# Kernel optimization log

Measured on AMD Instinct MI355X. Metric: run time of the kernel, lower is better.

The kernel has to match this reference:

```python
import jax, jax.numpy as jnp
import numpy as np

B, NG, NM, E, K, D = 1, 65536, 8192, 262144, 32, 128
EPS = 1e-5


def layernorm(x, g, b):
    mu = jnp.mean(x, axis=-1, keepdims=True)
    var = jnp.mean(jnp.square(x - mu), axis=-1, keepdims=True)
    return (x - mu) * jax.lax.rsqrt(var + EPS) * g + b


def mlp(x, W, g, b):
    # Linear (no bias) -> tanh -> LayerNorm, matching MLP module
    return layernorm(jnp.tanh(x @ W), g, b)


def setup_inputs() -> dict:
    key = jax.random.key(0)
    ks = jax.random.split(key, 16)
    inp = {
        "grid_mesh_bond_embedding": jax.random.normal(ks[0], (B, E, D), jnp.float32),
        "grid_rect_embedding": jax.random.normal(ks[1], (B, NG, D), jnp.float32),
        "mesh_node_embedding": jax.random.normal(ks[2], (B, NM, D), jnp.float32),
        "edge_id2pair": jnp.stack(
            [jax.random.randint(ks[3], (E,), 0, NG),
             jax.random.randint(ks[4], (E,), 0, NM)], axis=1),  # [E,2] int
        "edge_id_of_node": jax.random.randint(ks[5], (NM, K), 0, E),  # [NM,K] int
        "edge_coef": jax.random.uniform(ks[6], (NM, K, 1), jnp.float32),
        # MLP_G2M_GM2E: Linear(3D -> D), LayerNorm(D)
        "W_gm2e": jax.random.normal(ks[7], (3 * D, D), jnp.float32) / np.sqrt(3 * D),
        "g_gm2e": jnp.ones((D,), jnp.float32),
        "b_gm2e": jnp.zeros((D,), jnp.float32),
        # MLP_G2M_E2M: Linear(2D -> D), LayerNorm(D)
        "W_e2m": jax.random.normal(ks[8], (2 * D, D), jnp.float32) / np.sqrt(2 * D),
        "g_e2m": jnp.ones((D,), jnp.float32),
        "b_e2m": jnp.zeros((D,), jnp.float32),
        # MLP_G2M_G2G: Linear(D -> D), LayerNorm(D)
        "W_g2g": jax.random.normal(ks[9], (D, D), jnp.float32) / np.sqrt(D),
        "g_g2g": jnp.ones((D,), jnp.float32),
        "b_g2g": jnp.zeros((D,), jnp.float32),
    }
    return inp


def reference(grid_mesh_bond_embedding, grid_rect_embedding, mesh_node_embedding,
              edge_id2pair, edge_id_of_node, edge_coef,
              W_gm2e, g_gm2e, b_gm2e, W_e2m, g_e2m, b_e2m, W_g2g, g_g2g, b_g2g):
    # Edge update: gather rect/node endpoints, concat, MLP -> [B,E,D]
    rect_src = grid_rect_embedding[:, edge_id2pair[:, 0]]  # [B,E,D]
    node_dst = mesh_node_embedding[:, edge_id2pair[:, 1]]  # [B,E,D]
    edge_in = jnp.concatenate([grid_mesh_bond_embedding, rect_src, node_dst], axis=-1)
    delta_edge = mlp(edge_in, W_gm2e, g_gm2e, b_gm2e)  # [B,E,D]

    # Node update: gather K edges per mesh node, coef-weighted mean over K
    gathered = delta_edge[:, edge_id_of_node]  # [B,NM,K,D]
    agg = jnp.mean(gathered * edge_coef, axis=-2)  # [B,NM,D]
    delta_node = mlp(jnp.concatenate([mesh_node_embedding, agg], axis=-1), W_e2m, g_e2m, b_e2m)

    # Grid rect self-update
    delta_rect = mlp(grid_rect_embedding, W_g2g, g_g2g, b_g2g)

    return (grid_mesh_bond_embedding + delta_edge,
            grid_rect_embedding + delta_rect,
            mesh_node_embedding + delta_node)
```

## Files before the change

kernel.cpp:

```cpp
#include <hip/hip_runtime.h>


typedef __bf16 bf16x8 __attribute__((ext_vector_type(8)));
typedef __bf16 bf16x4 __attribute__((ext_vector_type(4)));
typedef float f32x4 __attribute__((ext_vector_type(4)));

#define E_CNT 262144
#define NG_CNT 65536
#define NM_CNT 8192

__device__ __forceinline__ float fast_tanh(float x) {
  float e = __expf(2.f * x);
  return 1.f - 2.f / (1.f + e);
}

template <int KDIM>
__device__ __forceinline__ void stage_W(const float* __restrict__ W, __bf16* wt) {
  constexpr int NCH = (KDIM / 32) * 8 * 64;
  for (int c = threadIdx.x; c < NCH; c += blockDim.x) {
    const int lane6 = c & 63, cx = lane6 & 15, qq = lane6 >> 4;
    const int kkn = c >> 6, kk = kkn >> 3, nn = kkn & 7;
    const int k0 = kk * 32 + qq * 8, col = nn * 16 + cx;
    bf16x8 v;
#pragma unroll
    for (int j = 0; j < 8; ++j) v[j] = (__bf16)W[(k0 + j) * 128 + col];
    *(bf16x8*)(wt + c * 8) = v;
  }
}

template <bool STORE_D>
__device__ __forceinline__ void mlp_epilogue(f32x4* acc, const f32x4* R,
                                             const float* gvec,
                                             const float* bvec, int q,
                                             float* op, __bf16* dp) {
  float s1 = 0.f, s2 = 0.f;
#pragma unroll
  for (int n = 0; n < 8; ++n)
#pragma unroll
    for (int j = 0; j < 4; ++j) {
      float v = fast_tanh(acc[n][j]);
      acc[n][j] = v;
      s1 += v;
      s2 += v * v;
    }
  s1 += __shfl_xor(s1, 16, 64);
  s2 += __shfl_xor(s2, 16, 64);
  s1 += __shfl_xor(s1, 32, 64);
  s2 += __shfl_xor(s2, 32, 64);
  const float mu = s1 * (1.f / 128.f);
  const float rs = rsqrtf(s2 * (1.f / 128.f) - mu * mu + 1e-5f);
#pragma unroll
  for (int n = 0; n < 8; ++n) {
    const f32x4 G = *(const f32x4*)(gvec + n * 16 + q * 4);
    const f32x4 Bv = *(const f32x4*)(bvec + n * 16 + q * 4);
    f32x4 o;
    bf16x4 db;
#pragma unroll
    for (int j = 0; j < 4; ++j) {
      const float d = (acc[n][j] - mu) * rs * G[j] + Bv[j];
      o[j] = R[n][j] + d;
      db[j] = (__bf16)d;
    }
    *(f32x4*)(op + n * 16 + q * 4) = o;
    if (STORE_D) *(bf16x4*)(dp + n * 16 + q * 4) = db;
  }
}

template <bool STORE_D>
__global__ __launch_bounds__(256) __attribute__((amdgpu_waves_per_eu(3, 4)))
void edge_kernel(const float* __restrict__ gm, const int* __restrict__ pair,
                 const __bf16* __restrict__ P1, const __bf16* __restrict__ P2,
                 const float* __restrict__ W, const float* __restrict__ gvec,
                 const float* __restrict__ bvec, float* __restrict__ out,
                 __bf16* __restrict__ delta_out, int M) {
  __shared__ __bf16 wt[2048 * 8];
  stage_W<128>(W, wt);
  __syncthreads();
  const int tid = threadIdx.x, lane = tid & 63, wid = tid >> 6;
  const int r = lane & 15, q = lane >> 4;
  const __bf16* wl = wt + lane * 8;
  const int t = blockIdx.x * 4 + wid;
  if (t >= (M >> 4)) return;
  const int row = (t << 4) + r;
  const float* pa = gm + (size_t)row * 128;

  f32x4 F[4][2];
#pragma unroll
  for (int kk = 0; kk < 4; ++kk) {
    F[kk][0] = *(const f32x4*)(pa + kk * 32 + q * 8);
    F[kk][1] = *(const f32x4*)(pa + kk * 32 + q * 8 + 4);
  }
  f32x4 R[8];
#pragma unroll
  for (int n = 0; n < 8; ++n) R[n] = *(const f32x4*)(pa + n * 16 + q * 4);
  const int2 sd = *(const int2*)(pair + 2 * (size_t)row);

  bf16x4 pg1[8], pg2[8];
  const __bf16* p1 = P1 + (size_t)sd.x * 128 + q * 4;
  const __bf16* p2 = P2 + (size_t)sd.y * 128 + q * 4;
#pragma unroll
  for (int n = 0; n < 8; ++n) {
    pg1[n] = *(const bf16x4*)(p1 + n * 16);
    pg2[n] = *(const bf16x4*)(p2 + n * 16);
  }

  bf16x8 ab[4];
#pragma unroll
  for (int kk = 0; kk < 4; ++kk)
#pragma unroll
    for (int j = 0; j < 4; ++j) {
      ab[kk][j] = (__bf16)F[kk][0][j];
      ab[kk][4 + j] = (__bf16)F[kk][1][j];
    }
  f32x4 acc[8];
#pragma unroll
  for (int n = 0; n < 8; ++n)
#pragma unroll
    for (int j = 0; j < 4; ++j)
      acc[n][j] = (float)pg1[n][j] + (float)pg2[n][j];
#pragma unroll
  for (int kk = 0; kk < 4; ++kk)
#pragma unroll
    for (int n = 0; n < 8; ++n)
      acc[n] = __builtin_amdgcn_mfma_f32_16x16x32_bf16(
          *(const bf16x8*)(wl + (kk * 8 + n) * 512), ab[kk], acc[n], 0, 0, 0);

  mlp_epilogue<STORE_D>(acc, R, gvec, bvec, q, out + (size_t)row * 128,
                        STORE_D ? delta_out + (size_t)row * 128 : nullptr);
}

__global__ __launch_bounds__(256) __attribute__((amdgpu_waves_per_eu(2, 4)))
void rect_fused_kernel(const float* __restrict__ rect,
                       const float* __restrict__ W1b,
                       const float* __restrict__ W3,
                       const float* __restrict__ gvec,
                       const float* __restrict__ bvec,
                       float* __restrict__ out1, __bf16* __restrict__ P1,
                       int M) {
  __shared__ __bf16 wt[4096 * 8];
  stage_W<128>(W1b, wt);
  stage_W<128>(W3, wt + 16384);
  __syncthreads();
  const int tid = threadIdx.x, lane = tid & 63, wid = tid >> 6;
  const int r = lane & 15, q = lane >> 4;
  const __bf16* wl = wt + lane * 8;
  const int t = blockIdx.x * 4 + wid;
  if (t >= (M >> 4)) return;
  const int row = (t << 4) + r;
  const float* pa = rect + (size_t)row * 128;

  f32x4 F[4][2];
#pragma unroll
  for (int kk = 0; kk < 4; ++kk) {
    F[kk][0] = *(const f32x4*)(pa + kk * 32 + q * 8);
    F[kk][1] = *(const f32x4*)(pa + kk * 32 + q * 8 + 4);
  }
  f32x4 R[8];
#pragma unroll
  for (int n = 0; n < 8; ++n) R[n] = *(const f32x4*)(pa + n * 16 + q * 4);

  bf16x8 ab[4];
#pragma unroll
  for (int kk = 0; kk < 4; ++kk)
#pragma unroll
    for (int j = 0; j < 4; ++j) {
      ab[kk][j] = (__bf16)F[kk][0][j];
      ab[kk][4 + j] = (__bf16)F[kk][1][j];
    }
  f32x4 acc[8] = {};
#pragma unroll
  for (int kk = 0; kk < 4; ++kk)
#pragma unroll
    for (int n = 0; n < 8; ++n)
      acc[n] = __builtin_amdgcn_mfma_f32_16x16x32_bf16(
          *(const bf16x8*)(wl + (kk * 8 + n) * 512), ab[kk], acc[n], 0, 0, 0);
  __bf16* pp = P1 + (size_t)row * 128;
#pragma unroll
  for (int n = 0; n < 8; ++n) {
    bf16x4 o;
#pragma unroll
    for (int j = 0; j < 4; ++j) o[j] = (__bf16)acc[n][j];
    *(bf16x4*)(pp + n * 16 + q * 4) = o;
  }
  f32x4 acc2[8] = {};
#pragma unroll
  for (int kk = 0; kk < 4; ++kk)
#pragma unroll
    for (int n = 0; n < 8; ++n)
      acc2[n] = __builtin_amdgcn_mfma_f32_16x16x32_bf16(
          *(const bf16x8*)(wl + 16384 + (kk * 8 + n) * 512), ab[kk], acc2[n], 0,
          0, 0);
  mlp_epilogue<false>(acc2, R, gvec, bvec, q, out1 + (size_t)row * 128, nullptr);
}

__global__ __launch_bounds__(256) __attribute__((amdgpu_waves_per_eu(3, 4)))
void mlp128_kernel(const float* __restrict__ A, const float* __restrict__ W,
                   const float* __restrict__ gvec, const float* __restrict__ bvec,
                   float* __restrict__ out, int M) {
  __shared__ __bf16 wt[2048 * 8];
  stage_W<128>(W, wt);
  __syncthreads();
  const int tid = threadIdx.x, lane = tid & 63, wid = tid >> 6;
  const int r = lane & 15, q = lane >> 4;
  const __bf16* wl = wt + lane * 8;
  const int t = blockIdx.x * 4 + wid;
  if (t >= (M >> 4)) return;
  const int row = (t << 4) + r;
  const float* pa = A + (size_t)row * 128;
  f32x4 F[4][2];
#pragma unroll
  for (int kk = 0; kk < 4; ++kk) {
    F[kk][0] = *(const f32x4*)(pa + kk * 32 + q * 8);
    F[kk][1] = *(const f32x4*)(pa + kk * 32 + q * 8 + 4);
  }
  f32x4 R[8];
#pragma unroll
  for (int n = 0; n < 8; ++n) R[n] = *(const f32x4*)(pa + n * 16 + q * 4);
  bf16x8 ab[4];
#pragma unroll
  for (int kk = 0; kk < 4; ++kk)
#pragma unroll
    for (int j = 0; j < 4; ++j) {
      ab[kk][j] = (__bf16)F[kk][0][j];
      ab[kk][4 + j] = (__bf16)F[kk][1][j];
    }
  f32x4 acc[8] = {};
#pragma unroll
  for (int kk = 0; kk < 4; ++kk)
#pragma unroll
    for (int n = 0; n < 8; ++n)
      acc[n] = __builtin_amdgcn_mfma_f32_16x16x32_bf16(
          *(const bf16x8*)(wl + (kk * 8 + n) * 512), ab[kk], acc[n], 0, 0, 0);
  mlp_epilogue<false>(acc, R, gvec, bvec, q, out + (size_t)row * 128, nullptr);
}

__global__ __launch_bounds__(256) __attribute__((amdgpu_waves_per_eu(3, 4)))
void lin_kernel(const float* __restrict__ A, const float* __restrict__ W,
                __bf16* __restrict__ out, int M) {
  __shared__ __bf16 wt[2048 * 8];
  stage_W<128>(W, wt);
  __syncthreads();
  const int tid = threadIdx.x, lane = tid & 63, wid = tid >> 6;
  const int r = lane & 15, q = lane >> 4;
  const __bf16* wl = wt + lane * 8;
  const int t = blockIdx.x * 4 + wid;
  if (t >= (M >> 4)) return;
  const int row = (t << 4) + r;
  const float* pa = A + (size_t)row * 128;
  f32x4 F[4][2];
#pragma unroll
  for (int kk = 0; kk < 4; ++kk) {
    F[kk][0] = *(const f32x4*)(pa + kk * 32 + q * 8);
    F[kk][1] = *(const f32x4*)(pa + kk * 32 + q * 8 + 4);
  }
  bf16x8 ab[4];
#pragma unroll
  for (int kk = 0; kk < 4; ++kk)
#pragma unroll
    for (int j = 0; j < 4; ++j) {
      ab[kk][j] = (__bf16)F[kk][0][j];
      ab[kk][4 + j] = (__bf16)F[kk][1][j];
    }
  f32x4 acc[8] = {};
#pragma unroll
  for (int kk = 0; kk < 4; ++kk)
#pragma unroll
    for (int n = 0; n < 8; ++n)
      acc[n] = __builtin_amdgcn_mfma_f32_16x16x32_bf16(
          *(const bf16x8*)(wl + (kk * 8 + n) * 512), ab[kk], acc[n], 0, 0, 0);
  __bf16* po = out + (size_t)row * 128;
#pragma unroll
  for (int n = 0; n < 8; ++n) {
    bf16x4 o;
#pragma unroll
    for (int j = 0; j < 4; ++j) o[j] = (__bf16)acc[n][j];
    *(bf16x4*)(po + n * 16 + q * 4) = o;
  }
}

__global__ __launch_bounds__(256) __attribute__((amdgpu_waves_per_eu(2, 4)))
void node_kernel(const __bf16* __restrict__ Ab, const float* __restrict__ W,
                 const float* __restrict__ gvec, const float* __restrict__ bvec,
                 const float* __restrict__ resid, float* __restrict__ out,
                 int M) {
  __shared__ __bf16 wt[4096 * 8];
  stage_W<256>(W, wt);
  __syncthreads();
  const int tid = threadIdx.x, lane = tid & 63, wid = tid >> 6;
  const int r = lane & 15, q = lane >> 4;
  const __bf16* wl = wt + lane * 8;
  const int t = blockIdx.x * 4 + wid;
  if (t >= (M >> 4)) return;
  const int row = (t << 4) + r;
  const __bf16* pb = Ab + (size_t)row * 256 + q * 8;
  bf16x8 ab[8];
#pragma unroll
  for (int kk = 0; kk < 8; ++kk) ab[kk] = *(const bf16x8*)(pb + kk * 32);
  f32x4 R[8];
#pragma unroll
  for (int n = 0; n < 8; ++n)
    R[n] = *(const f32x4*)(resid + (size_t)row * 128 + n * 16 + q * 4);
  f32x4 acc[8] = {};
#pragma unroll
  for (int kk = 0; kk < 8; ++kk)
#pragma unroll
    for (int n = 0; n < 8; ++n)
      acc[n] = __builtin_amdgcn_mfma_f32_16x16x32_bf16(
          *(const bf16x8*)(wl + (kk * 8 + n) * 512), ab[kk], acc[n], 0, 0, 0);
  mlp_epilogue<false>(acc, R, gvec, bvec, q, out + (size_t)row * 128, nullptr);
}

template <bool FROM_WS>
__global__ __launch_bounds__(256) void agg_kernel(
    const __bf16* __restrict__ dws, const float* __restrict__ out0,
    const float* __restrict__ gm, const float* __restrict__ mesh,
    const int* __restrict__ eid, const float* __restrict__ coef,
    __bf16* __restrict__ x2) {
  __shared__ int eid_s[512];
  __shared__ float cf_s[512];
  const int t = threadIdx.x;
  const int n0 = blockIdx.x * 16;
  for (int i = t; i < 512; i += 256) {
    eid_s[i] = eid[n0 * 32 + i];
    cf_s[i] = coef[n0 * 32 + i];
  }
  __syncthreads();
  const int rl = t >> 4;
  const int d8 = (t & 15) * 8;
  const int row = n0 + rl;
  float acc[8] = {0, 0, 0, 0, 0, 0, 0, 0};
  for (int k = 0; k < 32; ++k) {
    const int e = eid_s[rl * 32 + k];
    const float cf = cf_s[rl * 32 + k];
    if (FROM_WS) {
      bf16x8 v = *(const bf16x8*)(dws + (size_t)e * 128 + d8);
#pragma unroll
      for (int j = 0; j < 8; ++j) acc[j] += cf * (float)v[j];
    } else {
      const float* po = out0 + (size_t)e * 128 + d8;
      const float* pg = gm + (size_t)e * 128 + d8;
      f32x4 o0 = *(const f32x4*)po, o1 = *(const f32x4*)(po + 4);
      f32x4 g0 = *(const f32x4*)pg, g1 = *(const f32x4*)(pg + 4);
#pragma unroll
      for (int j = 0; j < 4; ++j) {
        acc[j] += cf * (o0[j] - g0[j]);
        acc[4 + j] += cf * (o1[j] - g1[j]);
      }
    }
  }
  const float* pm = mesh + (size_t)row * 128 + d8;
  f32x4 m0 = *(const f32x4*)pm, m1 = *(const f32x4*)(pm + 4);
  bf16x8 mv, av;
#pragma unroll
  for (int j = 0; j < 4; ++j) {
    mv[j] = (__bf16)m0[j];
    mv[4 + j] = (__bf16)m1[j];
  }
#pragma unroll
  for (int j = 0; j < 8; ++j) av[j] = (__bf16)(acc[j] * (1.0f / 32.0f));
  *(bf16x8*)(x2 + (size_t)row * 256 + d8) = mv;
  *(bf16x8*)(x2 + (size_t)row * 256 + 128 + d8) = av;
}

extern "C" void kernel_launch(void* const* d_in, const int* in_sizes, int n_in,
                              void* d_out, int out_size, void* d_ws,
                              size_t ws_size, hipStream_t stream) {
  const float* gm = (const float*)d_in[0];
  const float* rect = (const float*)d_in[1];
  const float* mesh = (const float*)d_in[2];
  const int* pair = (const int*)d_in[3];
  const int* eid = (const int*)d_in[4];
  const float* coef = (const float*)d_in[5];
  const float* W1 = (const float*)d_in[6];
  const float* g1 = (const float*)d_in[7];
  const float* b1 = (const float*)d_in[8];
  const float* W2 = (const float*)d_in[9];
  const float* g2 = (const float*)d_in[10];
  const float* b2 = (const float*)d_in[11];
  const float* W3 = (const float*)d_in[12];
  const float* g3 = (const float*)d_in[13];
  const float* b3 = (const float*)d_in[14];

  float* out0 = (float*)d_out;
  float* out1 = out0 + (size_t)E_CNT * 128;
  float* out2 = out1 + (size_t)NG_CNT * 128;

  const size_t deltaE = (size_t)E_CNT * 128;
  const size_t x2E = (size_t)NM_CNT * 256;
  const size_t p1E = (size_t)NG_CNT * 128;
  const bool fastD = ws_size >= (deltaE + x2E) * 2;
  const bool fastP = ws_size >= (deltaE + x2E + p1E) * 2;

  __bf16* delta = (__bf16*)d_ws;
  __bf16* x2 = fastD ? delta + deltaE : (__bf16*)d_ws;
  __bf16* P1ws = delta + deltaE + x2E;
  __bf16* P2 = (__bf16*)out2;

  const __bf16* P1;
  if (fastP) {
    rect_fused_kernel<<<1024, 256, 0, stream>>>(rect, W1 + 128 * 128, W3, g3,
                                                b3, out1, P1ws, NG_CNT);
    P1 = P1ws;
  } else {
    lin_kernel<<<1024, 256, 0, stream>>>(rect, W1 + 128 * 128, (__bf16*)out1,
                                         NG_CNT);
    P1 = (const __bf16*)out1;
  }
  lin_kernel<<<128, 256, 0, stream>>>(mesh, W1 + 256 * 128, P2, NM_CNT);

  if (fastD) {
    edge_kernel<true><<<4096, 256, 0, stream>>>(gm, pair, P1, P2, W1, g1, b1,
                                                out0, delta, E_CNT);
    agg_kernel<true><<<512, 256, 0, stream>>>(delta, nullptr, nullptr, mesh,
                                              eid, coef, x2);
  } else {
    edge_kernel<false><<<4096, 256, 0, stream>>>(gm, pair, P1, P2, W1, g1, b1,
                                                 out0, nullptr, E_CNT);
    agg_kernel<false><<<512, 256, 0, stream>>>(nullptr, out0, gm, mesh, eid,
                                               coef, x2);
  }
  if (!fastP) {
    mlp128_kernel<<<1024, 256, 0, stream>>>(rect, W3, g3, b3, out1, NG_CNT);
  }
  node_kernel<<<128, 256, 0, stream>>>(x2, W2, g2, b2, mesh, out2, NM_CNT);
}
```

Baseline: 208.6 us.

## Make MLP kernels persistent with grid-stride loops and prefetch edge gathers

Converts the edge, rect, mlp128 and lin kernels into grid-stride persistent loops and cuts their grid sizes, so the per-block weight staging into LDS is amortized over several tiles. The edge kernel also software-pipelines its indexed gathers: it loads the next tile's pair indices and P1/P2 rows while computing the current tile. It additionally uses nontemporal stores for the large fp32 edge output. The cost is fewer resident blocks, which may hide latency less well, plus extra register pressure from the prefetch buffers.

```diff
diff --git a/kernel.cpp b/kernel.cpp
--- a/kernel.cpp
+++ b/kernel.cpp
@@ -28,7 +28,7 @@
   }
 }
 
-template <bool STORE_D>
+template <bool STORE_D, bool NT>
 __device__ __forceinline__ void mlp_epilogue(f32x4* acc, const f32x4* R,
                                              const float* gvec,
                                              const float* bvec, int q,
@@ -61,7 +61,10 @@
       o[j] = R[n][j] + d;
       db[j] = (__bf16)d;
     }
-    *(f32x4*)(op + n * 16 + q * 4) = o;
+    if (NT)
+      __builtin_nontemporal_store(o, (f32x4*)(op + n * 16 + q * 4));
+    else
+      *(f32x4*)(op + n * 16 + q * 4) = o;
     if (STORE_D) *(bf16x4*)(dp + n * 16 + q * 4) = db;
   }
 }
@@ -79,54 +82,73 @@
   const int tid = threadIdx.x, lane = tid & 63, wid = tid >> 6;
   const int r = lane & 15, q = lane >> 4;
   const __bf16* wl = wt + lane * 8;
-  const int t = blockIdx.x * 4 + wid;
-  if (t >= (M >> 4)) return;
-  const int row = (t << 4) + r;
-  const float* pa = gm + (size_t)row * 128;
-
-  f32x4 F[4][2];
-#pragma unroll
-  for (int kk = 0; kk < 4; ++kk) {
-    F[kk][0] = *(const f32x4*)(pa + kk * 32 + q * 8);
-    F[kk][1] = *(const f32x4*)(pa + kk * 32 + q * 8 + 4);
-  }
-  f32x4 R[8];
-#pragma unroll
-  for (int n = 0; n < 8; ++n) R[n] = *(const f32x4*)(pa + n * 16 + q * 4);
-  const int2 sd = *(const int2*)(pair + 2 * (size_t)row);
-
+  const int nw = gridDim.x * 4;
+  const int tiles = M >> 4;
+  int t = blockIdx.x * 4 + wid;
+  if (t >= tiles) return;
+
+  int2 sd = *(const int2*)(pair + 2 * (size_t)((t << 4) + r));
   bf16x4 pg1[8], pg2[8];
-  const __bf16* p1 = P1 + (size_t)sd.x * 128 + q * 4;
-  const __bf16* p2 = P2 + (size_t)sd.y * 128 + q * 4;
-#pragma unroll
-  for (int n = 0; n < 8; ++n) {
-    pg1[n] = *(const bf16x4*)(p1 + n * 16);
-    pg2[n] = *(const bf16x4*)(p2 + n * 16);
-  }
-
-  bf16x8 ab[4];
-#pragma unroll
-  for (int kk = 0; kk < 4; ++kk)
-#pragma unroll
-    for (int j = 0; j < 4; ++j) {
-      ab[kk][j] = (__bf16)F[kk][0][j];
-      ab[kk][4 + j] = (__bf16)F[kk][1][j];
-    }
-  f32x4 acc[8];
-#pragma unroll
-  for (int n = 0; n < 8; ++n)
-#pragma unroll
-    for (int j = 0; j < 4; ++j)
-      acc[n][j] = (float)pg1[n][j] + (float)pg2[n][j];
-#pragma unroll
-  for (int kk = 0; kk < 4; ++kk)
+  {
+    const __bf16* p1 = P1 + (size_t)sd.x * 128 + q * 4;
+    const __bf16* p2 = P2 + (size_t)sd.y * 128 + q * 4;
+#pragma unroll
+    for (int n = 0; n < 8; ++n) {
+      pg1[n] = *(const bf16x4*)(p1 + n * 16);
+      pg2[n] = *(const bf16x4*)(p2 + n * 16);
+    }
+  }
+  int2 sd_next = {0, 0};
+  if (t + nw < tiles)
+    sd_next = *(const int2*)(pair + 2 * (size_t)(((t + nw) << 4) + r));
+
+  for (; t < tiles; t += nw) {
+    const int row = (t << 4) + r;
+    const float* pa = gm + (size_t)row * 128;
+    f32x4 F[4][2];
+#pragma unroll
+    for (int kk = 0; kk < 4; ++kk) {
+      F[kk][0] = *(const f32x4*)(pa + kk * 32 + q * 8);
+      F[kk][1] = *(const f32x4*)(pa + kk * 32 + q * 8 + 4);
+    }
+    f32x4 R[8];
+#pragma unroll
+    for (int n = 0; n < 8; ++n) R[n] = *(const f32x4*)(pa + n * 16 + q * 4);
+    f32x4 acc[8];
 #pragma unroll
     for (int n = 0; n < 8; ++n)
-      acc[n] = __builtin_amdgcn_mfma_f32_16x16x32_bf16(
-          *(const bf16x8*)(wl + (kk * 8 + n) * 512), ab[kk], acc[n], 0, 0, 0);
-
-  mlp_epilogue<STORE_D>(acc, R, gvec, bvec, q, out + (size_t)row * 128,
-                        STORE_D ? delta_out + (size_t)row * 128 : nullptr);
+#pragma unroll
+      for (int j = 0; j < 4; ++j)
+        acc[n][j] = (float)pg1[n][j] + (float)pg2[n][j];
+    if (t + nw < tiles) {
+      const __bf16* p1 = P1 + (size_t)sd_next.x * 128 + q * 4;
+      const __bf16* p2 = P2 + (size_t)sd_next.y * 128 + q * 4;
+#pragma unroll
+      for (int n = 0; n < 8; ++n) {
+        pg1[n] = *(const bf16x4*)(p1 + n * 16);
+        pg2[n] = *(const bf16x4*)(p2 + n * 16);
+      }
+      if (t + 2 * nw < tiles)
+        sd_next = *(const int2*)(pair + 2 * (size_t)(((t + 2 * nw) << 4) + r));
+    }
+    bf16x8 ab[4];
+#pragma unroll
+    for (int kk = 0; kk < 4; ++kk)
+#pragma unroll
+      for (int j = 0; j < 4; ++j) {
+        ab[kk][j] = (__bf16)F[kk][0][j];
+        ab[kk][4 + j] = (__bf16)F[kk][1][j];
+      }
+#pragma unroll
+    for (int kk = 0; kk < 4; ++kk)
+#pragma unroll
+      for (int n = 0; n < 8; ++n)
+        acc[n] = __builtin_amdgcn_mfma_f32_16x16x32_bf16(
+            *(const bf16x8*)(wl + (kk * 8 + n) * 512), ab[kk], acc[n], 0, 0, 0);
+    mlp_epilogue<STORE_D, true>(
+        acc, R, gvec, bvec, q, out + (size_t)row * 128,
+        STORE_D ? delta_out + (size_t)row * 128 : nullptr);
+  }
 }
 
 __global__ __launch_bounds__(256) __attribute__((amdgpu_waves_per_eu(2, 4)))
@@ -144,53 +166,54 @@
   const int tid = threadIdx.x, lane = tid & 63, wid = tid >> 6;
   const int r = lane & 15, q = lane >> 4;
   const __bf16* wl = wt + lane * 8;
-  const int t = blockIdx.x * 4 + wid;
-  if (t >= (M >> 4)) return;
-  const int row = (t << 4) + r;
-  const float* pa = rect + (size_t)row * 128;
-
-  f32x4 F[4][2];
-#pragma unroll
-  for (int kk = 0; kk < 4; ++kk) {
-    F[kk][0] = *(const f32x4*)(pa + kk * 32 + q * 8);
-    F[kk][1] = *(const f32x4*)(pa + kk * 32 + q * 8 + 4);
-  }
-  f32x4 R[8];
-#pragma unroll
-  for (int n = 0; n < 8; ++n) R[n] = *(const f32x4*)(pa + n * 16 + q * 4);
-
-  bf16x8 ab[4];
-#pragma unroll
-  for (int kk = 0; kk < 4; ++kk)
-#pragma unroll
-    for (int j = 0; j < 4; ++j) {
-      ab[kk][j] = (__bf16)F[kk][0][j];
-      ab[kk][4 + j] = (__bf16)F[kk][1][j];
-    }
-  f32x4 acc[8] = {};
-#pragma unroll
-  for (int kk = 0; kk < 4; ++kk)
-#pragma unroll
-    for (int n = 0; n < 8; ++n)
-      acc[n] = __builtin_amdgcn_mfma_f32_16x16x32_bf16(
-          *(const bf16x8*)(wl + (kk * 8 + n) * 512), ab[kk], acc[n], 0, 0, 0);
-  __bf16* pp = P1 + (size_t)row * 128;
-#pragma unroll
-  for (int n = 0; n < 8; ++n) {
-    bf16x4 o;
-#pragma unroll
-    for (int j = 0; j < 4; ++j) o[j] = (__bf16)acc[n][j];
-    *(bf16x4*)(pp + n * 16 + q * 4) = o;
-  }
-  f32x4 acc2[8] = {};
-#pragma unroll
-  for (int kk = 0; kk < 4; ++kk)
-#pragma unroll
-    for (int n = 0; n < 8; ++n)
-      acc2[n] = __builtin_amdgcn_mfma_f32_16x16x32_bf16(
-          *(const bf16x8*)(wl + 16384 + (kk * 8 + n) * 512), ab[kk], acc2[n], 0,
-          0, 0);
-  mlp_epilogue<false>(acc2, R, gvec, bvec, q, out1 + (size_t)row * 128, nullptr);
+  const int nw = gridDim.x * 4;
+  const int tiles = M >> 4;
+  for (int t = blockIdx.x * 4 + wid; t < tiles; t += nw) {
+    const int row = (t << 4) + r;
+    const float* pa = rect + (size_t)row * 128;
+    f32x4 F[4][2];
+#pragma unroll
+    for (int kk = 0; kk < 4; ++kk) {
+      F[kk][0] = *(const f32x4*)(pa + kk * 32 + q * 8);
+      F[kk][1] = *(const f32x4*)(pa + kk * 32 + q * 8 + 4);
+    }
+    f32x4 R[8];
+#pragma unroll
+    for (int n = 0; n < 8; ++n) R[n] = *(const f32x4*)(pa + n * 16 + q * 4);
+    bf16x8 ab[4];
+#pragma unroll
+    for (int kk = 0; kk < 4; ++kk)
+#pragma unroll
+      for (int j = 0; j < 4; ++j) {
+        ab[kk][j] = (__bf16)F[kk][0][j];
+        ab[kk][4 + j] = (__bf16)F[kk][1][j];
+      }
+    f32x4 acc[8] = {};
+#pragma unroll
+    for (int kk = 0; kk < 4; ++kk)
+#pragma unroll
+      for (int n = 0; n < 8; ++n)
+        acc[n] = __builtin_amdgcn_mfma_f32_16x16x32_bf16(
+            *(const bf16x8*)(wl + (kk * 8 + n) * 512), ab[kk], acc[n], 0, 0, 0);
+    __bf16* pp = P1 + (size_t)row * 128;
+#pragma unroll
+    for (int n = 0; n < 8; ++n) {
+      bf16x4 o;
+#pragma unroll
+      for (int j = 0; j < 4; ++j) o[j] = (__bf16)acc[n][j];
+      *(bf16x4*)(pp + n * 16 + q * 4) = o;
+    }
+    f32x4 acc2[8] = {};
+#pragma unroll
+    for (int kk = 0; kk < 4; ++kk)
+#pragma unroll
+      for (int n = 0; n < 8; ++n)
+        acc2[n] = __builtin_amdgcn_mfma_f32_16x16x32_bf16(
+            *(const bf16x8*)(wl + 16384 + (kk * 8 + n) * 512), ab[kk], acc2[n],
+            0, 0, 0);
+    mlp_epilogue<false, false>(acc2, R, gvec, bvec, q,
+                               out1 + (size_t)row * 128, nullptr);
+  }
 }
 
 __global__ __launch_bounds__(256) __attribute__((amdgpu_waves_per_eu(3, 4)))
@@ -203,35 +226,38 @@
   const int tid = threadIdx.x, lane = tid & 63, wid = tid >> 6;
   const int r = lane & 15, q = lane >> 4;
   const __bf16* wl = wt + lane * 8;
-  const int t = blockIdx.x * 4 + wid;
-  if (t >= (M >> 4)) return;
-  const int row = (t << 4) + r;
-  const float* pa = A + (size_t)row * 128;
-  f32x4 F[4][2];
-#pragma unroll
-  for (int kk = 0; kk < 4; ++kk) {
-    F[kk][0] = *(const f32x4*)(pa + kk * 32 + q * 8);
-    F[kk][1] = *(const f32x4*)(pa + kk * 32 + q * 8 + 4);
-  }
-  f32x4 R[8];
-#pragma unroll
-  for (int n = 0; n < 8; ++n) R[n] = *(const f32x4*)(pa + n * 16 + q * 4);
-  bf16x8 ab[4];
-#pragma unroll
-  for (int kk = 0; kk < 4; ++kk)
-#pragma unroll
-    for (int j = 0; j < 4; ++j) {
-      ab[kk][j] = (__bf16)F[kk][0][j];
-      ab[kk][4 + j] = (__bf16)F[kk][1][j];
-    }
-  f32x4 acc[8] = {};
-#pragma unroll
-  for (int kk = 0; kk < 4; ++kk)
-#pragma unroll
-    for (int n = 0; n < 8; ++n)
-      acc[n] = __builtin_amdgcn_mfma_f32_16x16x32_bf16(
-          *(const bf16x8*)(wl + (kk * 8 + n) * 512), ab[kk], acc[n], 0, 0, 0);
-  mlp_epilogue<false>(acc, R, gvec, bvec, q, out + (size_t)row * 128, nullptr);
+  const int nw = gridDim.x * 4;
+  const int tiles = M >> 4;
+  for (int t = blockIdx.x * 4 + wid; t < tiles; t += nw) {
+    const int row = (t << 4) + r;
+    const float* pa = A + (size_t)row * 128;
+    f32x4 F[4][2];
+#pragma unroll
+    for (int kk = 0; kk < 4; ++kk) {
+      F[kk][0] = *(const f32x4*)(pa + kk * 32 + q * 8);
+      F[kk][1] = *(const f32x4*)(pa + kk * 32 + q * 8 + 4);
+    }
+    f32x4 R[8];
+#pragma unroll
+    for (int n = 0; n < 8; ++n) R[n] = *(const f32x4*)(pa + n * 16 + q * 4);
+    bf16x8 ab[4];
+#pragma unroll
+    for (int kk = 0; kk < 4; ++kk)
+#pragma unroll
+      for (int j = 0; j < 4; ++j) {
+        ab[kk][j] = (__bf16)F[kk][0][j];
+        ab[kk][4 + j] = (__bf16)F[kk][1][j];
+      }
+    f32x4 acc[8] = {};
+#pragma unroll
+    for (int kk = 0; kk < 4; ++kk)
+#pragma unroll
+      for (int n = 0; n < 8; ++n)
+        acc[n] = __builtin_amdgcn_mfma_f32_16x16x32_bf16(
+            *(const bf16x8*)(wl + (kk * 8 + n) * 512), ab[kk], acc[n], 0, 0, 0);
+    mlp_epilogue<false, false>(acc, R, gvec, bvec, q, out + (size_t)row * 128,
+                               nullptr);
+  }
 }
 
 __global__ __launch_bounds__(256) __attribute__((amdgpu_waves_per_eu(3, 4)))
@@ -243,38 +269,40 @@
   const int tid = threadIdx.x, lane = tid & 63, wid = tid >> 6;
   const int r = lane & 15, q = lane >> 4;
   const __bf16* wl = wt + lane * 8;
-  const int t = blockIdx.x * 4 + wid;
-  if (t >= (M >> 4)) return;
-  const int row = (t << 4) + r;
-  const float* pa = A + (size_t)row * 128;
-  f32x4 F[4][2];
-#pragma unroll
-  for (int kk = 0; kk < 4; ++kk) {
-    F[kk][0] = *(const f32x4*)(pa + kk * 32 + q * 8);
-    F[kk][1] = *(const f32x4*)(pa + kk * 32 + q * 8 + 4);
-  }
-  bf16x8 ab[4];
-#pragma unroll
-  for (int kk = 0; kk < 4; ++kk)
-#pragma unroll
-    for (int j = 0; j < 4; ++j) {
-      ab[kk][j] = (__bf16)F[kk][0][j];
-      ab[kk][4 + j] = (__bf16)F[kk][1][j];
-    }
-  f32x4 acc[8] = {};
-#pragma unroll
-  for (int kk = 0; kk < 4; ++kk)
-#pragma unroll
-    for (int n = 0; n < 8; ++n)
-      acc[n] = __builtin_amdgcn_mfma_f32_16x16x32_bf16(
-          *(const bf16x8*)(wl + (kk * 8 + n) * 512), ab[kk], acc[n], 0, 0, 0);
-  __bf16* po = out + (size_t)row * 128;
-#pragma unroll
-  for (int n = 0; n < 8; ++n) {
-    bf16x4 o;
-#pragma unroll
-    for (int j = 0; j < 4; ++j) o[j] = (__bf16)acc[n][j];
-    *(bf16x4*)(po + n * 16 + q * 4) = o;
+  const int nw = gridDim.x * 4;
+  const int tiles = M >> 4;
+  for (int t = blockIdx.x * 4 + wid; t < tiles; t += nw) {
+    const int row = (t << 4) + r;
+    const float* pa = A + (size_t)row * 128;
+    f32x4 F[4][2];
+#pragma unroll
+    for (int kk = 0; kk < 4; ++kk) {
+      F[kk][0] = *(const f32x4*)(pa + kk * 32 + q * 8);
+      F[kk][1] = *(const f32x4*)(pa + kk * 32 + q * 8 + 4);
+    }
+    bf16x8 ab[4];
+#pragma unroll
+    for (int kk = 0; kk < 4; ++kk)
+#pragma unroll
+      for (int j = 0; j < 4; ++j) {
+        ab[kk][j] = (__bf16)F[kk][0][j];
+        ab[kk][4 + j] = (__bf16)F[kk][1][j];
+      }
+    f32x4 acc[8] = {};
+#pragma unroll
+    for (int kk = 0; kk < 4; ++kk)
+#pragma unroll
+      for (int n = 0; n < 8; ++n)
+        acc[n] = __builtin_amdgcn_mfma_f32_16x16x32_bf16(
+            *(const bf16x8*)(wl + (kk * 8 + n) * 512), ab[kk], acc[n], 0, 0, 0);
+    __bf16* po = out + (size_t)row * 128;
+#pragma unroll
+    for (int n = 0; n < 8; ++n) {
+      bf16x4 o;
+#pragma unroll
+      for (int j = 0; j < 4; ++j) o[j] = (__bf16)acc[n][j];
+      *(bf16x4*)(po + n * 16 + q * 4) = o;
+    }
   }
 }
 
@@ -307,7 +335,8 @@
     for (int n = 0; n < 8; ++n)
       acc[n] = __builtin_amdgcn_mfma_f32_16x16x32_bf16(
           *(const bf16x8*)(wl + (kk * 8 + n) * 512), ab[kk], acc[n], 0, 0, 0);
-  mlp_epilogue<false>(acc, R, gvec, bvec, q, out + (size_t)row * 128, nullptr);
+  mlp_epilogue<false, false>(acc, R, gvec, bvec, q, out + (size_t)row * 128,
+                             nullptr);
 }
 
 template <bool FROM_WS>
@@ -398,29 +427,29 @@
 
   const __bf16* P1;
   if (fastP) {
-    rect_fused_kernel<<<1024, 256, 0, stream>>>(rect, W1 + 128 * 128, W3, g3,
-                                                b3, out1, P1ws, NG_CNT);
+    rect_fused_kernel<<<256, 256, 0, stream>>>(rect, W1 + 128 * 128, W3, g3,
+                                               b3, out1, P1ws, NG_CNT);
     P1 = P1ws;
   } else {
-    lin_kernel<<<1024, 256, 0, stream>>>(rect, W1 + 128 * 128, (__bf16*)out1,
-                                         NG_CNT);
+    lin_kernel<<<256, 256, 0, stream>>>(rect, W1 + 128 * 128, (__bf16*)out1,
+                                        NG_CNT);
     P1 = (const __bf16*)out1;
   }
   lin_kernel<<<128, 256, 0, stream>>>(mesh, W1 + 256 * 128, P2, NM_CNT);
 
   if (fastD) {
-    edge_kernel<true><<<4096, 256, 0, stream>>>(gm, pair, P1, P2, W1, g1, b1,
+    edge_kernel<true><<<1024, 256, 0, stream>>>(gm, pair, P1, P2, W1, g1, b1,
                                                 out0, delta, E_CNT);
     agg_kernel<true><<<512, 256, 0, stream>>>(delta, nullptr, nullptr, mesh,
                                               eid, coef, x2);
   } else {
-    edge_kernel<false><<<4096, 256, 0, stream>>>(gm, pair, P1, P2, W1, g1, b1,
+    edge_kernel<false><<<1024, 256, 0, stream>>>(gm, pair, P1, P2, W1, g1, b1,
                                                  out0, nullptr, E_CNT);
     agg_kernel<false><<<512, 256, 0, stream>>>(nullptr, out0, gm, mesh, eid,
                                                coef, x2);
   }
   if (!fastP) {
-    mlp128_kernel<<<1024, 256, 0, stream>>>(rect, W3, g3, b3, out1, NG_CNT);
+    mlp128_kernel<<<256, 256, 0, stream>>>(rect, W3, g3, b3, out1, NG_CNT);
   }
   node_kernel<<<128, 256, 0, stream>>>(x2, W2, g2, b2, mesh, out2, NM_CNT);
 }
```

Result: slower. 442.2 us (+112.1%).

## Pre-convert weights to bf16 MFMA layout once and process two tiles per wave

Applied to the files above, without the earlier changes.

Adds a small kernel that converts all three weight matrices once into the bf16 fragment layout in workspace. Each kernel then stages its weights with plain vector copies instead of strided fp32 gathers and per-block conversion. The edge and rect kernels now handle two 16-row tiles per wave with half the blocks, which halves how often weights are staged and lets the second tile's gathers overlap the first tile's compute. The trade-off is one extra launch, higher register pressure from dropping the waves_per_eu hints and holding two tiles of gathered data, and workspace space carved from the end of the buffer.

```diff
diff --git a/kernel.cpp b/kernel.cpp
--- a/kernel.cpp
+++ b/kernel.cpp
@@ -4,28 +4,51 @@
 typedef __bf16 bf16x8 __attribute__((ext_vector_type(8)));
 typedef __bf16 bf16x4 __attribute__((ext_vector_type(4)));
 typedef float f32x4 __attribute__((ext_vector_type(4)));
+typedef unsigned int u32x4 __attribute__((ext_vector_type(4)));
 
 #define E_CNT 262144
 #define NG_CNT 65536
 #define NM_CNT 8192
 
+#define WF_A 0
+#define WF_B 16384
+#define WF_C 32768
+#define WF_3 49152
+#define WF_2 65536
+#define WF_TOT 98304
+
 __device__ __forceinline__ float fast_tanh(float x) {
   float e = __expf(2.f * x);
   return 1.f - 2.f / (1.f + e);
 }
 
-template <int KDIM>
-__device__ __forceinline__ void stage_W(const float* __restrict__ W, __bf16* wt) {
-  constexpr int NCH = (KDIM / 32) * 8 * 64;
-  for (int c = threadIdx.x; c < NCH; c += blockDim.x) {
-    const int lane6 = c & 63, cx = lane6 & 15, qq = lane6 >> 4;
-    const int kkn = c >> 6, kk = kkn >> 3, nn = kkn & 7;
-    const int k0 = kk * 32 + qq * 8, col = nn * 16 + cx;
-    bf16x8 v;
-#pragma unroll
-    for (int j = 0; j < 8; ++j) v[j] = (__bf16)W[(k0 + j) * 128 + col];
-    *(bf16x8*)(wt + c * 8) = v;
-  }
+__global__ __launch_bounds__(256) void convert_w_kernel(
+    const float* __restrict__ W1, const float* __restrict__ W2,
+    const float* __restrict__ W3, __bf16* __restrict__ WF) {
+  const int cid = blockIdx.x * 256 + threadIdx.x;
+  if (cid >= 12288) return;
+  const float* src;
+  __bf16* dst;
+  int local;
+  if (cid < 2048) { src = W1; local = cid; dst = WF + WF_A; }
+  else if (cid < 4096) { src = W1 + 128 * 128; local = cid - 2048; dst = WF + WF_B; }
+  else if (cid < 6144) { src = W1 + 256 * 128; local = cid - 4096; dst = WF + WF_C; }
+  else if (cid < 8192) { src = W3; local = cid - 6144; dst = WF + WF_3; }
+  else { src = W2; local = cid - 8192; dst = WF + WF_2; }
+  const int lane6 = local & 63, cx = lane6 & 15, qq = lane6 >> 4;
+  const int kkn = local >> 6, kk = kkn >> 3, nn = kkn & 7;
+  const int k0 = kk * 32 + qq * 8, col = nn * 16 + cx;
+  bf16x8 v;
+#pragma unroll
+  for (int j = 0; j < 8; ++j) v[j] = (__bf16)src[(k0 + j) * 128 + col];
+  *(bf16x8*)(dst + local * 8) = v;
+}
+
+__device__ __forceinline__ void stage_copy(const __bf16* __restrict__ wf,
+                                           __bf16* wt, int nelems) {
+  const int n16 = nelems >> 3;
+  for (int i = threadIdx.x; i < n16; i += blockDim.x)
+    *(u32x4*)(wt + i * 8) = *(const u32x4*)(wf + i * 8);
 }
 
 template <bool STORE_D>
@@ -67,43 +90,49 @@
 }
 
 template <bool STORE_D>
-__global__ __launch_bounds__(256) __attribute__((amdgpu_waves_per_eu(3, 4)))
-void edge_kernel(const float* __restrict__ gm, const int* __restrict__ pair,
-                 const __bf16* __restrict__ P1, const __bf16* __restrict__ P2,
-                 const float* __restrict__ W, const float* __restrict__ gvec,
-                 const float* __restrict__ bvec, float* __restrict__ out,
-                 __bf16* __restrict__ delta_out, int M) {
-  __shared__ __bf16 wt[2048 * 8];
-  stage_W<128>(W, wt);
+__global__ __launch_bounds__(256) void edge_kernel(
+    const float* __restrict__ gm, const int* __restrict__ pair,
+    const __bf16* __restrict__ P1, const __bf16* __restrict__ P2,
+    const __bf16* __restrict__ WF, const float* __restrict__ gvec,
+    const float* __restrict__ bvec, float* __restrict__ out,
+    __bf16* __restrict__ delta_out) {
+  __shared__ __bf16 wt[16384];
+  stage_copy(WF, wt, 16384);
   __syncthreads();
   const int tid = threadIdx.x, lane = tid & 63, wid = tid >> 6;
   const int r = lane & 15, q = lane >> 4;
   const __bf16* wl = wt + lane * 8;
-  const int t = blockIdx.x * 4 + wid;
-  if (t >= (M >> 4)) return;
-  const int row = (t << 4) + r;
-  const float* pa = gm + (size_t)row * 128;
-
+  const int row0 = ((blockIdx.x * 8 + wid) << 4) + r;
+  const int row1 = row0 + 64;
+
+  const int2 sd0 = *(const int2*)(pair + 2 * (size_t)row0);
+  const int2 sd1 = *(const int2*)(pair + 2 * (size_t)row1);
+  const float* pa0 = gm + (size_t)row0 * 128;
   f32x4 F[4][2];
 #pragma unroll
   for (int kk = 0; kk < 4; ++kk) {
-    F[kk][0] = *(const f32x4*)(pa + kk * 32 + q * 8);
-    F[kk][1] = *(const f32x4*)(pa + kk * 32 + q * 8 + 4);
-  }
-  f32x4 R[8];
-#pragma unroll
-  for (int n = 0; n < 8; ++n) R[n] = *(const f32x4*)(pa + n * 16 + q * 4);
-  const int2 sd = *(const int2*)(pair + 2 * (size_t)row);
-
-  bf16x4 pg1[8], pg2[8];
-  const __bf16* p1 = P1 + (size_t)sd.x * 128 + q * 4;
-  const __bf16* p2 = P2 + (size_t)sd.y * 128 + q * 4;
-#pragma unroll
-  for (int n = 0; n < 8; ++n) {
-    pg1[n] = *(const bf16x4*)(p1 + n * 16);
-    pg2[n] = *(const bf16x4*)(p2 + n * 16);
-  }
-
+    F[kk][0] = *(const f32x4*)(pa0 + kk * 32 + q * 8);
+    F[kk][1] = *(const f32x4*)(pa0 + kk * 32 + q * 8 + 4);
+  }
+  bf16x4 gA1[8], gA2[8], gB1[8], gB2[8];
+  {
+    const __bf16* p1 = P1 + (size_t)sd0.x * 128 + q * 4;
+    const __bf16* p2 = P2 + (size_t)sd0.y * 128 + q * 4;
+#pragma unroll
+    for (int n = 0; n < 8; ++n) {
+      gA1[n] = *(const bf16x4*)(p1 + n * 16);
+      gA2[n] = *(const bf16x4*)(p2 + n * 16);
+    }
+  }
+  {
+    const __bf16* p1 = P1 + (size_t)sd1.x * 128 + q * 4;
+    const __bf16* p2 = P2 + (size_t)sd1.y * 128 + q * 4;
+#pragma unroll
+    for (int n = 0; n < 8; ++n) {
+      gB1[n] = *(const bf16x4*)(p1 + n * 16);
+      gB2[n] = *(const bf16x4*)(p2 + n * 16);
+    }
+  }
   bf16x8 ab[4];
 #pragma unroll
   for (int kk = 0; kk < 4; ++kk)
@@ -112,93 +141,120 @@
       ab[kk][j] = (__bf16)F[kk][0][j];
       ab[kk][4 + j] = (__bf16)F[kk][1][j];
     }
+  const float* pa1 = gm + (size_t)row1 * 128;
+  f32x4 F1[4][2];
+#pragma unroll
+  for (int kk = 0; kk < 4; ++kk) {
+    F1[kk][0] = *(const f32x4*)(pa1 + kk * 32 + q * 8);
+    F1[kk][1] = *(const f32x4*)(pa1 + kk * 32 + q * 8 + 4);
+  }
   f32x4 acc[8];
 #pragma unroll
   for (int n = 0; n < 8; ++n)
 #pragma unroll
-    for (int j = 0; j < 4; ++j)
-      acc[n][j] = (float)pg1[n][j] + (float)pg2[n][j];
+    for (int j = 0; j < 4; ++j) acc[n][j] = (float)gA1[n][j] + (float)gA2[n][j];
 #pragma unroll
   for (int kk = 0; kk < 4; ++kk)
 #pragma unroll
     for (int n = 0; n < 8; ++n)
       acc[n] = __builtin_amdgcn_mfma_f32_16x16x32_bf16(
           *(const bf16x8*)(wl + (kk * 8 + n) * 512), ab[kk], acc[n], 0, 0, 0);
-
-  mlp_epilogue<STORE_D>(acc, R, gvec, bvec, q, out + (size_t)row * 128,
-                        STORE_D ? delta_out + (size_t)row * 128 : nullptr);
-}
-
-__global__ __launch_bounds__(256) __attribute__((amdgpu_waves_per_eu(2, 4)))
-void rect_fused_kernel(const float* __restrict__ rect,
-                       const float* __restrict__ W1b,
-                       const float* __restrict__ W3,
-                       const float* __restrict__ gvec,
-                       const float* __restrict__ bvec,
-                       float* __restrict__ out1, __bf16* __restrict__ P1,
-                       int M) {
-  __shared__ __bf16 wt[4096 * 8];
-  stage_W<128>(W1b, wt);
-  stage_W<128>(W3, wt + 16384);
+  f32x4 R[8];
+#pragma unroll
+  for (int n = 0; n < 8; ++n) R[n] = *(const f32x4*)(pa0 + n * 16 + q * 4);
+  mlp_epilogue<STORE_D>(acc, R, gvec, bvec, q, out + (size_t)row0 * 128,
+                        STORE_D ? delta_out + (size_t)row0 * 128 : nullptr);
+#pragma unroll
+  for (int kk = 0; kk < 4; ++kk)
+#pragma unroll
+    for (int j = 0; j < 4; ++j) {
+      ab[kk][j] = (__bf16)F1[kk][0][j];
+      ab[kk][4 + j] = (__bf16)F1[kk][1][j];
+    }
+#pragma unroll
+  for (int n = 0; n < 8; ++n)
+#pragma unroll
+    for (int j = 0; j < 4; ++j) acc[n][j] = (float)gB1[n][j] + (float)gB2[n][j];
+#pragma unroll
+  for (int kk = 0; kk < 4; ++kk)
+#pragma unroll
+    for (int n = 0; n < 8; ++n)
+      acc[n] = __builtin_amdgcn_mfma_f32_16x16x32_bf16(
+          *(const bf16x8*)(wl + (kk * 8 + n) * 512), ab[kk], acc[n], 0, 0, 0);
+#pragma unroll
+  for (int n = 0; n < 8; ++n) R[n] = *(const f32x4*)(pa1 + n * 16 + q * 4);
+  mlp_epilogue<STORE_D>(acc, R, gvec, bvec, q, out + (size_t)row1 * 128,
+                        STORE_D ? delta_out + (size_t)row1 * 128 : nullptr);
+}
+
+__global__ __launch_bounds__(256) void rect_fused_kernel(
+    const float* __restrict__ rect, const __bf16* __restrict__ WFb,
+    const __bf16* __restrict__ WF3, const float* __restrict__ gvec,
+    const float* __restrict__ bvec, float* __restrict__ out1,
+    __bf16* __restrict__ P1) {
+  __shared__ __bf16 wt[32768];
+  stage_copy(WFb, wt, 16384);
+  stage_copy(WF3, wt + 16384, 16384);
   __syncthreads();
   const int tid = threadIdx.x, lane = tid & 63, wid = tid >> 6;
   const int r = lane & 15, q = lane >> 4;
   const __bf16* wl = wt + lane * 8;
-  const int t = blockIdx.x * 4 + wid;
-  if (t >= (M >> 4)) return;
-  const int row = (t << 4) + r;
-  const float* pa = rect + (size_t)row * 128;
-
-  f32x4 F[4][2];
-#pragma unroll
-  for (int kk = 0; kk < 4; ++kk) {
-    F[kk][0] = *(const f32x4*)(pa + kk * 32 + q * 8);
-    F[kk][1] = *(const f32x4*)(pa + kk * 32 + q * 8 + 4);
-  }
-  f32x4 R[8];
-#pragma unroll
-  for (int n = 0; n < 8; ++n) R[n] = *(const f32x4*)(pa + n * 16 + q * 4);
-
-  bf16x8 ab[4];
-#pragma unroll
-  for (int kk = 0; kk < 4; ++kk)
-#pragma unroll
-    for (int j = 0; j < 4; ++j) {
-      ab[kk][j] = (__bf16)F[kk][0][j];
-      ab[kk][4 + j] = (__bf16)F[kk][1][j];
-    }
-  f32x4 acc[8] = {};
-#pragma unroll
-  for (int kk = 0; kk < 4; ++kk)
-#pragma unroll
-    for (int n = 0; n < 8; ++n)
-      acc[n] = __builtin_amdgcn_mfma_f32_16x16x32_bf16(
-          *(const bf16x8*)(wl + (kk * 8 + n) * 512), ab[kk], acc[n], 0, 0, 0);
-  __bf16* pp = P1 + (size_t)row * 128;
-#pragma unroll
-  for (int n = 0; n < 8; ++n) {
-    bf16x4 o;
-#pragma unroll
-    for (int j = 0; j < 4; ++j) o[j] = (__bf16)acc[n][j];
-    *(bf16x4*)(pp + n * 16 + q * 4) = o;
-  }
-  f32x4 acc2[8] = {};
-#pragma unroll
-  for (int kk = 0; kk < 4; ++kk)
-#pragma unroll
-    for (int n = 0; n < 8; ++n)
-      acc2[n] = __builtin_amdgcn_mfma_f32_16x16x32_bf16(
-          *(const bf16x8*)(wl + 16384 + (kk * 8 + n) * 512), ab[kk], acc2[n], 0,
-          0, 0);
-  mlp_epilogue<false>(acc2, R, gvec, bvec, q, out1 + (size_t)row * 128, nullptr);
-}
-
-__global__ __launch_bounds__(256) __attribute__((amdgpu_waves_per_eu(3, 4)))
-void mlp128_kernel(const float* __restrict__ A, const float* __restrict__ W,
-                   const float* __restrict__ gvec, const float* __restrict__ bvec,
-                   float* __restrict__ out, int M) {
-  __shared__ __bf16 wt[2048 * 8];
-  stage_W<128>(W, wt);
+  const int row0 = ((blockIdx.x * 8 + wid) << 4) + r;
+#pragma unroll 1
+  for (int half = 0; half < 2; ++half) {
+    const int row = row0 + half * 64;
+    const float* pa = rect + (size_t)row * 128;
+    f32x4 F[4][2];
+#pragma unroll
+    for (int kk = 0; kk < 4; ++kk) {
+      F[kk][0] = *(const f32x4*)(pa + kk * 32 + q * 8);
+      F[kk][1] = *(const f32x4*)(pa + kk * 32 + q * 8 + 4);
+    }
+    bf16x8 ab[4];
+#pragma unroll
+    for (int kk = 0; kk < 4; ++kk)
+#pragma unroll
+      for (int j = 0; j < 4; ++j) {
+        ab[kk][j] = (__bf16)F[kk][0][j];
+        ab[kk][4 + j] = (__bf16)F[kk][1][j];
+      }
+    f32x4 acc[8] = {};
+#pragma unroll
+    for (int kk = 0; kk < 4; ++kk)
+#pragma unroll
+      for (int n = 0; n < 8; ++n)
+        acc[n] = __builtin_amdgcn_mfma_f32_16x16x32_bf16(
+            *(const bf16x8*)(wl + (kk * 8 + n) * 512), ab[kk], acc[n], 0, 0, 0);
+    __bf16* pp = P1 + (size_t)row * 128;
+#pragma unroll
+    for (int n = 0; n < 8; ++n) {
+      bf16x4 o;
+#pragma unroll
+      for (int j = 0; j < 4; ++j) o[j] = (__bf16)acc[n][j];
+      *(bf16x4*)(pp + n * 16 + q * 4) = o;
+    }
+    f32x4 acc2[8] = {};
+#pragma unroll
+    for (int kk = 0; kk < 4; ++kk)
+#pragma unroll
+      for (int n = 0; n < 8; ++n)
+        acc2[n] = __builtin_amdgcn_mfma_f32_16x16x32_bf16(
+            *(const bf16x8*)(wl + 16384 + (kk * 8 + n) * 512), ab[kk], acc2[n],
+            0, 0, 0);
+    f32x4 R[8];
+#pragma unroll
+    for (int n = 0; n < 8; ++n) R[n] = *(const f32x4*)(pa + n * 16 + q * 4);
+    mlp_epilogue<false>(acc2, R, gvec, bvec, q, out1 + (size_t)row * 128,
+                        nullptr);
+  }
+}
+
+__global__ __launch_bounds__(256) void mlp128_kernel(
+    const float* __restrict__ A, const __bf16* __restrict__ WFx,
+    const float* __restrict__ gvec, const float* __restrict__ bvec,
+    float* __restrict__ out, int M) {
+  __shared__ __bf16 wt[16384];
+  stage_copy(WFx, wt, 16384);
   __syncthreads();
   const int tid = threadIdx.x, lane = tid & 63, wid = tid >> 6;
   const int r = lane & 15, q = lane >> 4;
@@ -213,9 +269,6 @@
     F[kk][0] = *(const f32x4*)(pa + kk * 32 + q * 8);
     F[kk][1] = *(const f32x4*)(pa + kk * 32 + q * 8 + 4);
   }
-  f32x4 R[8];
-#pragma unroll
-  for (int n = 0; n < 8; ++n) R[n] = *(const f32x4*)(pa + n * 16 + q * 4);
   bf16x8 ab[4];
 #pragma unroll
   for (int kk = 0; kk < 4; ++kk)
@@ -231,14 +284,17 @@
     for (int n = 0; n < 8; ++n)
       acc[n] = __builtin_amdgcn_mfma_f32_16x16x32_bf16(
           *(const bf16x8*)(wl + (kk * 8 + n) * 512), ab[kk], acc[n], 0, 0, 0);
+  f32x4 R[8];
+#pragma unroll
+  for (int n = 0; n < 8; ++n) R[n] = *(const f32x4*)(pa + n * 16 + q * 4);
   mlp_epilogue<false>(acc, R, gvec, bvec, q, out + (size_t)row * 128, nullptr);
 }
 
-__global__ __launch_bounds__(256) __attribute__((amdgpu_waves_per_eu(3, 4)))
-void lin_kernel(const float* __restrict__ A, const float* __restrict__ W,
-                __bf16* __restrict__ out, int M) {
-  __shared__ __bf16 wt[2048 * 8];
-  stage_W<128>(W, wt);
+__global__ __launch_bounds__(256) void lin_kernel(
+    const float* __restrict__ A, const __bf16* __restrict__ WFx,
+    __bf16* __restrict__ out, int M) {
+  __shared__ __bf16 wt[16384];
+  stage_copy(WFx, wt, 16384);
   __syncthreads();
   const int tid = threadIdx.x, lane = tid & 63, wid = tid >> 6;
   const int r = lane & 15, q = lane >> 4;
@@ -278,13 +334,12 @@
   }
 }
 
-__global__ __launch_bounds__(256) __attribute__((amdgpu_waves_per_eu(2, 4)))
-void node_kernel(const __bf16* __restrict__ Ab, const float* __restrict__ W,
-                 const float* __restrict__ gvec, const float* __restrict__ bvec,
-                 const float* __restrict__ resid, float* __restrict__ out,
-                 int M) {
-  __shared__ __bf16 wt[4096 * 8];
-  stage_W<256>(W, wt);
+__global__ __launch_bounds__(256) void node_kernel(
+    const __bf16* __restrict__ Ab, const __bf16* __restrict__ WF2,
+    const float* __restrict__ gvec, const float* __restrict__ bvec,
+    const float* __restrict__ resid, float* __restrict__ out, int M) {
+  __shared__ __bf16 wt[32768];
+  stage_copy(WF2, wt, 32768);
   __syncthreads();
   const int tid = threadIdx.x, lane = tid & 63, wid = tid >> 6;
   const int r = lane & 15, q = lane >> 4;
@@ -385,42 +440,50 @@
   float* out1 = out0 + (size_t)E_CNT * 128;
   float* out2 = out1 + (size_t)NG_CNT * 128;
 
+  const size_t wfBytes = (size_t)WF_TOT * 2;
+  const size_t wfoff = (ws_size - wfBytes) & ~(size_t)63;
+  __bf16* WF = (__bf16*)((char*)d_ws + wfoff);
+
   const size_t deltaE = (size_t)E_CNT * 128;
   const size_t x2E = (size_t)NM_CNT * 256;
   const size_t p1E = (size_t)NG_CNT * 128;
-  const bool fastD = ws_size >= (deltaE + x2E) * 2;
-  const bool fastP = ws_size >= (deltaE + x2E + p1E) * 2;
+  const bool fastD = wfoff >= (deltaE + x2E) * 2;
+  const bool fastP = wfoff >= (deltaE + x2E + p1E) * 2;
 
   __bf16* delta = (__bf16*)d_ws;
   __bf16* x2 = fastD ? delta + deltaE : (__bf16*)d_ws;
   __bf16* P1ws = delta + deltaE + x2E;
   __bf16* P2 = (__bf16*)out2;
 
+  convert_w_kernel<<<48, 256, 0, stream>>>(W1, W2, W3, WF);
+
   const __bf16* P1;
   if (fastP) {
-    rect_fused_kernel<<<1024, 256, 0, stream>>>(rect, W1 + 128 * 128, W3, g3,
-                                                b3, out1, P1ws, NG_CNT);
+    rect_fused_kernel<<<512, 256, 0, stream>>>(rect, WF + WF_B, WF + WF_3, g3,
+                                               b3, out1, P1ws);
     P1 = P1ws;
   } else {
-    lin_kernel<<<1024, 256, 0, stream>>>(rect, W1 + 128 * 128, (__bf16*)out1,
+    lin_kernel<<<1024, 256, 0, stream>>>(rect, WF + WF_B, (__bf16*)out1,
                                          NG_CNT);
     P1 = (const __bf16*)out1;
   }
-  lin_kernel<<<128, 256, 0, stream>>>(mesh, W1 + 256 * 128, P2, NM_CNT);
+  lin_kernel<<<128, 256, 0, stream>>>(mesh, WF + WF_C, P2, NM_CNT);
 
   if (fastD) {
-    edge_kernel<true><<<4096, 256, 0, stream>>>(gm, pair, P1, P2, W1, g1, b1,
-                                                out0, delta, E_CNT);
+    edge_kernel<true><<<2048, 256, 0, stream>>>(gm, pair, P1, P2, WF + WF_A,
+                                                g1, b1, out0, delta);
     agg_kernel<true><<<512, 256, 0, stream>>>(delta, nullptr, nullptr, mesh,
                                               eid, coef, x2);
   } else {
-    edge_kernel<false><<<4096, 256, 0, stream>>>(gm, pair, P1, P2, W1, g1, b1,
-                                                 out0, nullptr, E_CNT);
+    edge_kernel<false><<<2048, 256, 0, stream>>>(gm, pair, P1, P2, WF + WF_A,
+                                                 g1, b1, out0, nullptr);
     agg_kernel<false><<<512, 256, 0, stream>>>(nullptr, out0, gm, mesh, eid,
                                                coef, x2);
   }
   if (!fastP) {
-    mlp128_kernel<<<1024, 256, 0, stream>>>(rect, W3, g3, b3, out1, NG_CNT);
-  }
-  node_kernel<<<128, 256, 0, stream>>>(x2, W2, g2, b2, mesh, out2, NM_CNT);
-}
+    mlp128_kernel<<<1024, 256, 0, stream>>>(rect, WF + WF_3, g3, b3, out1,
+                                            NG_CNT);
+  }
+  node_kernel<<<128, 256, 0, stream>>>(x2, WF + WF_2, g2, b2, mesh, out2,
+                                       NM_CNT);
+}
```

New measurement: 226.3 us. 8.5% more time.
